# Kernel tuning notes

Measured on AMD Instinct MI355X. Metric: run time of the kernel, lower is better.

Reference implementation:

```python
import jax, jax.numpy as jnp
import numpy as np

D_MODEL, D_STATE, D_INNER, DT_RANK, K = 64, 16, 128, 4, 4
EPS = 1e-6  # RMSNorm eps


def setup_inputs() -> dict:
    key = jax.random.key(0)
    ks = jax.random.split(key, 12)
    B, L = 8, 4096
    s = 0.02
    x = jax.random.normal(ks[0], (B, L, D_MODEL), dtype=jnp.float32)
    w_norm = jnp.ones((D_MODEL,), jnp.float32)
    W_in = jax.random.normal(ks[1], (2 * D_INNER, D_MODEL), jnp.float32) * s
    b_in = jnp.zeros((2 * D_INNER,), jnp.float32)
    W_conv = jax.random.normal(ks[2], (D_INNER, D_INNER, K), jnp.float32) * s
    b_conv = jnp.zeros((D_INNER,), jnp.float32)
    W_xp = jax.random.normal(ks[3], (DT_RANK + 2 * D_STATE, D_INNER), jnp.float32) * s
    b_xp = jnp.zeros((DT_RANK + 2 * D_STATE,), jnp.float32)
    W_dt = jax.random.normal(ks[4], (D_INNER, DT_RANK), jnp.float32) * s
    b_dt = jnp.zeros((D_INNER,), jnp.float32)
    W_out = jax.random.normal(ks[5], (D_MODEL, D_INNER), jnp.float32) * s
    b_out = jnp.zeros((D_MODEL,), jnp.float32)
    A_log = jnp.log(jnp.tile(jnp.arange(1, D_STATE + 1, dtype=jnp.float32), (D_INNER, 1)))
    D_param = jnp.ones((D_INNER,), jnp.float32)
    return dict(x=x, w_norm=w_norm, W_in=W_in, b_in=b_in, W_conv=W_conv, b_conv=b_conv,
                W_xp=W_xp, b_xp=b_xp, W_dt=W_dt, b_dt=b_dt, W_out=W_out, b_out=b_out,
                A_log=A_log, D_param=D_param)


def _mamba_block(xn, W_in, b_in, W_conv, b_conv, W_xp, b_xp, W_dt, b_dt, W_out, b_out, A_log, D_param):
    B, L, _ = xn.shape
    xz = xn @ W_in.T + b_in                      # (B,L,2*d_inner)
    u, z = jnp.split(xz, 2, axis=-1)
    z = jax.nn.silu(z)
    # conv1d: NCH, causal-style pad (K-1) both sides then truncate to L
    uc = jax.lax.conv_general_dilated(
        u.transpose(0, 2, 1), W_conv, window_strides=(1,), padding=[(K - 1, K - 1)],
        dimension_numbers=("NCH", "OIH", "NCH"))[:, :, :L] + b_conv[None, :, None]
    u = jax.nn.silu(uc.transpose(0, 2, 1))       # (B,L,d_inner)
    xp = u @ W_xp.T + b_xp
    dt, Bm, Cm = jnp.split(xp, [DT_RANK, DT_RANK + D_STATE], axis=-1)
    delta = jax.nn.softplus(dt @ W_dt.T + b_dt)  # (B,L,d_inner)
    A = -jnp.exp(A_log)                          # (d_inner, n)
    A_bar = jnp.exp(jnp.einsum('bld,dn->bldn', delta, A))
    B_bar_x = jnp.einsum('bld,bln,bld->bldn', delta, Bm, u)

    def step(h, inp):
        a, bx, c = inp                           # (B,d,n),(B,d,n),(B,n)
        h = a * h + bx
        y = jnp.einsum('bdn,bn->bd', h, c)
        return h, y

    h0 = jnp.zeros((B, D_INNER, D_STATE), xn.dtype)
    xs = (A_bar.transpose(1, 0, 2, 3), B_bar_x.transpose(1, 0, 2, 3), Cm.transpose(1, 0, 2))
    _, ys = jax.lax.scan(step, h0, xs)           # (L,B,d_inner)
    y = ys.transpose(1, 0, 2) + D_param * u
    y = y * z
    return y @ W_out.T + b_out


def reference(x, w_norm, W_in, b_in, W_conv, b_conv, W_xp, b_xp, W_dt, b_dt, W_out, b_out, A_log, D_param):
    xn = x * jax.lax.rsqrt(jnp.mean(x * x, axis=-1, keepdims=True) + EPS) * w_norm
    return x + _mamba_block(xn, W_in, b_in, W_conv, b_conv, W_xp, b_xp, W_dt, b_dt, W_out, b_out, A_log, D_param)
```

## Files before the change

### kernel.cpp

```cpp
#include <hip/hip_runtime.h>
#include <math.h>

#define D_MODEL 64
#define D_STATE 16
#define D_INNER 128
#define DT_RANK 4
#define BB 8
#define LL 4096
#define NTOK (BB*LL)
#define EPSV 1e-6f
#define NCHUNK 64
#define LC (LL/NCHUNK)
#define PAD 136

typedef __attribute__((ext_vector_type(8))) short bf16x8;
typedef __attribute__((ext_vector_type(4))) float f32x4;

__device__ __forceinline__ float sig_(float v) { return 1.f / (1.f + __expf(-v)); }
__device__ __forceinline__ float softplus_(float v) {
    return (v > 20.f) ? v : __logf(1.f + __expf(v));
}
__device__ __forceinline__ unsigned short f2bf(float x) {
    unsigned int u = __float_as_uint(x);
    u += 0x7fff + ((u >> 16) & 1);
    return (unsigned short)(u >> 16);
}
__device__ __forceinline__ float bf2f(unsigned short u) {
    return __uint_as_float(((unsigned int)u) << 16);
}
__device__ __forceinline__ unsigned int pack2bf(float a, float b) {
    return (unsigned int)f2bf(a) | ((unsigned int)f2bf(b) << 16);
}

__global__ __launch_bounds__(256) void pack_all(
    const float* __restrict__ W_in, const float* __restrict__ w_norm,
    const float* __restrict__ W_conv, const float* __restrict__ W_xp,
    const float* __restrict__ W_out,
    unsigned short* __restrict__ Win_bf, unsigned short* __restrict__ Bp,
    unsigned short* __restrict__ Wxp_bf, unsigned short* __restrict__ Wout_bf)
{
    int i = blockIdx.x * 256 + threadIdx.x;
    if (i < 16384) {
        Win_bf[i] = f2bf(W_in[i] * w_norm[i & 63]);
    } else if (i < 81920) {
        int j = i - 16384;
        int kk = j >> 14, o = (j >> 7) & 127, c = j & 127;
        Bp[j] = f2bf(W_conv[o * 512 + c * 4 + kk]);
    } else if (i < 88064) {
        int j = i - 81920;
        Wxp_bf[j] = ((j >> 7) < 36) ? f2bf(W_xp[j]) : (unsigned short)0;
    } else if (i < 96256) {
        int j = i - 88064;
        Wout_bf[j] = f2bf(W_out[j]);
    }
}

__global__ __launch_bounds__(256) void k123a_fused(
    const float* __restrict__ x, const unsigned short* __restrict__ Win_bf,
    const float* __restrict__ b_in,
    const unsigned short* __restrict__ Bp, const float* __restrict__ b_conv,
    const unsigned short* __restrict__ Wxp_bf, const float* __restrict__ b_xp,
    const float* __restrict__ W_dt, const float* __restrict__ b_dt,
    const float* __restrict__ A_log,
    unsigned short* __restrict__ z_bf, unsigned short* __restrict__ u_cbf,
    unsigned short* __restrict__ delta_bf,
    float* __restrict__ Bm, float* __restrict__ Cm,
    float* __restrict__ P, float* __restrict__ Q)
{
    __shared__ unsigned char smem[54832];
    unsigned short* axs  = (unsigned short*)smem;
    unsigned short* upre = (unsigned short*)(smem + 11520);
    unsigned short* dls  = upre;
    unsigned short* uls  = (unsigned short*)(smem + 29744);
    float* bls = (float*)(smem + 47152);
    float (*dts)[4] = (float(*)[4])(smem + 51248);
    float* Wd  = (float*)(smem + 52272);
    float* bds = (float*)(smem + 54320);

    int tid = threadIdx.x;
    if (tid < 128) *(float4*)&Wd[tid * 4] = *(const float4*)&W_dt[tid * 4];
    else if (tid < 160) *(float4*)&bds[(tid - 128) * 4] = *(const float4*)&b_dt[(tid - 128) * 4];
    int wave = tid >> 6, lane = tid & 63;
    int quad = lane >> 4, l16 = lane & 15;
    int tb = blockIdx.x * 64;
    int bbase = tb & ~4095;

    #pragma unroll
    for (int p = 0; p < 2; ++p) {
        int lrow = p * 64 + (tid >> 2);
        if (lrow < 67) {
            int qt = tid & 3;
            int g = tb - 3 + lrow;
            float4 v[4];
            float ss = 0.f;
            if (g >= bbase) {
                #pragma unroll
                for (int j = 0; j < 4; ++j) {
                    v[j] = *(const float4*)&x[g * 64 + qt * 16 + j * 4];
                    ss += v[j].x*v[j].x + v[j].y*v[j].y + v[j].z*v[j].z + v[j].w*v[j].w;
                }
            } else {
                #pragma unroll
                for (int j = 0; j < 4; ++j) v[j] = (float4){0.f, 0.f, 0.f, 0.f};
            }
            ss += __shfl_xor(ss, 1, 64);
            ss += __shfl_xor(ss, 2, 64);
            float r = rsqrtf(ss * (1.f / 64.f) + EPSV);
            unsigned short tmp[16];
            #pragma unroll
            for (int j = 0; j < 4; ++j) {
                tmp[4*j+0] = f2bf(v[j].x * r); tmp[4*j+1] = f2bf(v[j].y * r);
                tmp[4*j+2] = f2bf(v[j].z * r); tmp[4*j+3] = f2bf(v[j].w * r);
            }
            *(bf16x8*)&axs[lrow * 72 + qt * 16]     = *(bf16x8*)&tmp[0];
            *(bf16x8*)&axs[lrow * 72 + qt * 16 + 8] = *(bf16x8*)&tmp[8];
        }
    }
    __syncthreads();
    #pragma unroll
    for (int mt = 0; mt < 5; ++mt) {
        bf16x8 a0 = *(const bf16x8*)&axs[(mt * 16 + l16) * 72 + quad * 8];
        bf16x8 a1 = *(const bf16x8*)&axs[(mt * 16 + l16) * 72 + 32 + quad * 8];
        f32x4 acc[4];
        #pragma unroll
        for (int nk = 0; nk < 4; ++nk) acc[nk] = (f32x4){0.f, 0.f, 0.f, 0.f};
        #pragma unroll
        for (int nk = 0; nk < 4; ++nk) {
            int nt = wave * 4 + nk;
            bf16x8 b0 = *(const bf16x8*)&Win_bf[(nt * 16 + l16) * 64 + quad * 8];
            bf16x8 b1 = *(const bf16x8*)&Win_bf[(nt * 16 + l16) * 64 + 32 + quad * 8];
            acc[nk] = __builtin_amdgcn_mfma_f32_16x16x32_bf16(a0, b0, acc[nk], 0, 0, 0);
            acc[nk] = __builtin_amdgcn_mfma_f32_16x16x32_bf16(a1, b1, acc[nk], 0, 0, 0);
        }
        #pragma unroll
        for (int nk = 0; nk < 4; ++nk) {
            int o = (wave * 4 + nk) * 16 + l16;
            float bo = b_in[o];
            #pragma unroll
            for (int r = 0; r < 4; ++r) {
                int lrow = mt * 16 + quad * 4 + r;
                if (lrow < 67) {
                    float v = acc[nk][r] + bo;
                    if (o < 128) {
                        upre[lrow * PAD + o] = f2bf(v);
                    } else if (lrow >= 3) {
                        float zv = v * sig_(v);
                        z_bf[(tb + lrow - 3) * 128 + (o - 128)] = f2bf(zv);
                    }
                }
            }
        }
    }
    __syncthreads();
    {
        f32x4 acc[8];
        #pragma unroll
        for (int og = 0; og < 8; ++og) acc[og] = (f32x4){0.f, 0.f, 0.f, 0.f};
        #pragma unroll
        for (int kk = 0; kk < 4; ++kk) {
            int lr = wave * 16 + l16 + kk;
            #pragma unroll
            for (int cs = 0; cs < 4; ++cs) {
                int kbase = cs * 32 + quad * 8;
                bf16x8 a = *(const bf16x8*)&upre[lr * PAD + kbase];
                #pragma unroll
                for (int og = 0; og < 8; ++og) {
                    bf16x8 b = *(const bf16x8*)&Bp[kk * 16384 + (og * 16 + l16) * 128 + kbase];
                    acc[og] = __builtin_amdgcn_mfma_f32_16x16x32_bf16(a, b, acc[og], 0, 0, 0);
                }
            }
        }
        #pragma unroll
        for (int og = 0; og < 8; ++og) {
            int o = og * 16 + l16;
            float bc = b_conv[o];
            #pragma unroll
            for (int r = 0; r < 4; ++r) {
                int tloc = wave * 16 + quad * 4 + r;
                float v = acc[og][r] + bc;
                unsigned short ub = f2bf(v * sig_(v));
                u_cbf[(tb + tloc) * 128 + o] = ub;
                uls[tloc * PAD + o] = ub;
            }
        }
    }
    __syncthreads();
    {
        f32x4 xacc[3];
        #pragma unroll
        for (int nt = 0; nt < 3; ++nt) xacc[nt] = (f32x4){0.f, 0.f, 0.f, 0.f};
        #pragma unroll
        for (int cs = 0; cs < 4; ++cs) {
            int kbase = cs * 32 + quad * 8;
            bf16x8 a = *(const bf16x8*)&uls[(wave * 16 + l16) * PAD + kbase];
            #pragma unroll
            for (int nt = 0; nt < 3; ++nt) {
                bf16x8 b = *(const bf16x8*)&Wxp_bf[(nt * 16 + l16) * 128 + kbase];
                xacc[nt] = __builtin_amdgcn_mfma_f32_16x16x32_bf16(a, b, xacc[nt], 0, 0, 0);
            }
        }
        #pragma unroll
        for (int nt = 0; nt < 3; ++nt) {
            int j = nt * 16 + l16;
            float bx = (j < 36) ? b_xp[j] : 0.f;
            #pragma unroll
            for (int r = 0; r < 4; ++r) {
                int tloc = wave * 16 + quad * 4 + r;
                int t = tb + tloc;
                float val = xacc[nt][r] + bx;
                if (j < 4) {
                    dts[tloc][j] = val;
                } else if (j < 20) {
                    Bm[t * 16 + (j - 4)] = val;
                    bls[tloc * 16 + (j - 4)] = val;
                } else if (j < 36) {
                    Cm[t * 16 + (j - 20)] = val;
                }
            }
        }
    }
    __syncthreads();
    {
        int tokloc = tid >> 2, dgrp = tid & 3;
        float dt0 = dts[tokloc][0], dt1 = dts[tokloc][1],
              dt2 = dts[tokloc][2], dt3 = dts[tokloc][3];
        int g = tb + tokloc;
        #pragma unroll
        for (int d4 = 0; d4 < 8; ++d4) {
            int d = dgrp * 32 + d4 * 4;
            float4 w0 = *(const float4*)&Wd[(d + 0) * 4];
            float4 w1 = *(const float4*)&Wd[(d + 1) * 4];
            float4 w2 = *(const float4*)&Wd[(d + 2) * 4];
            float4 w3 = *(const float4*)&Wd[(d + 3) * 4];
            float4 bdv = *(const float4*)&bds[d];
            float4 r;
            r.x = softplus_(bdv.x + dt0*w0.x + dt1*w0.y + dt2*w0.z + dt3*w0.w);
            r.y = softplus_(bdv.y + dt0*w1.x + dt1*w1.y + dt2*w1.z + dt3*w1.w);
            r.z = softplus_(bdv.z + dt0*w2.x + dt1*w2.y + dt2*w2.z + dt3*w2.w);
            r.w = softplus_(bdv.w + dt0*w3.x + dt1*w3.y + dt2*w3.z + dt3*w3.w);
            uint2 pk; pk.x = pack2bf(r.x, r.y); pk.y = pack2bf(r.z, r.w);
            *(uint2*)&delta_bf[g * 128 + d] = pk;
            *(uint2*)&dls[tokloc * PAD + d] = pk;
        }
    }
    __syncthreads();
    {
        int d = tid >> 1;
        int nb = (tid & 1) * 8;
        float4 Av0 = *(const float4*)&A_log[d * 16 + nb];
        float4 Av1 = *(const float4*)&A_log[d * 16 + nb + 4];
        float A0 = -__expf(Av0.x), A1 = -__expf(Av0.y),
              A2 = -__expf(Av0.z), A3 = -__expf(Av0.w);
        float A4 = -__expf(Av1.x), A5 = -__expf(Av1.y),
              A6 = -__expf(Av1.z), A7 = -__expf(Av1.w);
        float P0=1.f,P1=1.f,P2=1.f,P3=1.f,P4=1.f,P5=1.f,P6=1.f,P7=1.f;
        float Q0=0.f,Q1=0.f,Q2=0.f,Q3=0.f,Q4=0.f,Q5=0.f,Q6=0.f,Q7=0.f;
        for (int t = 0; t < LC; ++t) {
            float dl = bf2f(dls[t * PAD + d]);
            float uu = bf2f(uls[t * PAD + d]);
            float4 bm0 = *(const float4*)&bls[t * 16 + nb];
            float4 bm1 = *(const float4*)&bls[t * 16 + nb + 4];
            float du = dl * uu;
            float a0 = __expf(dl * A0), a1 = __expf(dl * A1),
                  a2 = __expf(dl * A2), a3 = __expf(dl * A3);
            float a4 = __expf(dl * A4), a5 = __expf(dl * A5),
                  a6 = __expf(dl * A6), a7 = __expf(dl * A7);
            P0 *= a0; P1 *= a1; P2 *= a2; P3 *= a3;
            P4 *= a4; P5 *= a5; P6 *= a6; P7 *= a7;
            Q0 = a0 * Q0 + du * bm0.x; Q1 = a1 * Q1 + du * bm0.y;
            Q2 = a2 * Q2 + du * bm0.z; Q3 = a3 * Q3 + du * bm0.w;
            Q4 = a4 * Q4 + du * bm1.x; Q5 = a5 * Q5 + du * bm1.y;
            Q6 = a6 * Q6 + du * bm1.z; Q7 = a7 * Q7 + du * bm1.w;
        }
        int idx = blockIdx.x * 2048 + d * 16 + nb;
        *(float4*)&P[idx]     = (float4){P0, P1, P2, P3};
        *(float4*)&P[idx + 4] = (float4){P4, P5, P6, P7};
        *(float4*)&Q[idx]     = (float4){Q0, Q1, Q2, Q3};
        *(float4*)&Q[idx + 4] = (float4){Q4, Q5, Q6, Q7};
    }
}

__global__ __launch_bounds__(256) void k4b_carry(
    const float* __restrict__ P, const float* __restrict__ Q, float* __restrict__ Hinit)
{
    int tid = blockIdx.x * 256 + threadIdx.x;
    int b = tid >> 11, dn = tid & 2047;
    float carry = 0.f;
    for (int c0 = 0; c0 < NCHUNK; c0 += 8) {
        float p[8], q[8];
        #pragma unroll
        for (int j = 0; j < 8; ++j) {
            int idx = (b * NCHUNK + c0 + j) * 2048 + dn;
            p[j] = P[idx]; q[j] = Q[idx];
        }
        #pragma unroll
        for (int j = 0; j < 8; ++j) {
            int idx = (b * NCHUNK + c0 + j) * 2048 + dn;
            Hinit[idx] = carry;
            carry = p[j] * carry + q[j];
        }
    }
}

__global__ __launch_bounds__(256) void k4c5_fused(
    const unsigned short* __restrict__ delta_bf, const unsigned short* __restrict__ u_cbf,
    const float* __restrict__ Bm, const float* __restrict__ Cm,
    const unsigned short* __restrict__ z_bf, const float* __restrict__ A_log,
    const float* __restrict__ D_param, const float* __restrict__ Hinit,
    const unsigned short* __restrict__ Wout_bf, const float* __restrict__ b_out,
    const float* __restrict__ x, float* __restrict__ out)
{
    __shared__ unsigned short dls[LC * 128];
    __shared__ unsigned short uls[LC * 128];
    __shared__ float bls[LC * 16];
    __shared__ float cls[LC * 16];
    __shared__ unsigned short yzls[LC * PAD];
    int bid = blockIdx.x;
    int tid = threadIdx.x, lane = tid & 63;
    int g0 = bid * 64;
    for (int i = tid; i < LC * 16; i += 256) {
        int row = i >> 4, q = i & 15;
        *(float4*)&dls[row * 128 + q * 8] =
            *(const float4*)&delta_bf[(g0 + row) * 128 + q * 8];
        *(float4*)&uls[row * 128 + q * 8] =
            *(const float4*)&u_cbf[(g0 + row) * 128 + q * 8];
        *(float4*)&yzls[row * PAD + q * 8] =
            *(const float4*)&z_bf[(g0 + row) * 128 + q * 8];
    }
    for (int i = tid; i < LC * 4; i += 256) {
        int row = i >> 2, q = i & 3;
        *(float4*)&bls[row * 16 + q * 4] = *(const float4*)&Bm[(g0 + row) * 16 + q * 4];
        *(float4*)&cls[row * 16 + q * 4] = *(const float4*)&Cm[(g0 + row) * 16 + q * 4];
    }
    int d = tid >> 1;
    int nb = (tid & 1) * 8;
    float4 Av0 = *(const float4*)&A_log[d * 16 + nb];
    float4 Av1 = *(const float4*)&A_log[d * 16 + nb + 4];
    float A0 = -__expf(Av0.x), A1 = -__expf(Av0.y), A2 = -__expf(Av0.z), A3 = -__expf(Av0.w);
    float A4 = -__expf(Av1.x), A5 = -__expf(Av1.y), A6 = -__expf(Av1.z), A7 = -__expf(Av1.w);
    int hbase = bid * 2048 + d * 16 + nb;
    float4 h0 = *(const float4*)&Hinit[hbase];
    float4 h1 = *(const float4*)&Hinit[hbase + 4];
    float Dp = D_param[d];
    __syncthreads();
    for (int t = 0; t < LC; ++t) {
        float dl = bf2f(dls[t * 128 + d]);
        float uu = bf2f(uls[t * 128 + d]);
        float4 bm0 = *(const float4*)&bls[t * 16 + nb];
        float4 bm1 = *(const float4*)&bls[t * 16 + nb + 4];
        float4 cm0 = *(const float4*)&cls[t * 16 + nb];
        float4 cm1 = *(const float4*)&cls[t * 16 + nb + 4];
        float du = dl * uu;
        float a0 = __expf(dl * A0), a1 = __expf(dl * A1),
              a2 = __expf(dl * A2), a3 = __expf(dl * A3);
        float a4 = __expf(dl * A4), a5 = __expf(dl * A5),
              a6 = __expf(dl * A6), a7 = __expf(dl * A7);
        h0.x = a0 * h0.x + du * bm0.x; h0.y = a1 * h0.y + du * bm0.y;
        h0.z = a2 * h0.z + du * bm0.z; h0.w = a3 * h0.w + du * bm0.w;
        h1.x = a4 * h1.x + du * bm1.x; h1.y = a5 * h1.y + du * bm1.y;
        h1.z = a6 * h1.z + du * bm1.z; h1.w = a7 * h1.w + du * bm1.w;
        float yv = h0.x * cm0.x + h0.y * cm0.y + h0.z * cm0.z + h0.w * cm0.w
                 + h1.x * cm1.x + h1.y * cm1.y + h1.z * cm1.z + h1.w * cm1.w;
        yv += __shfl_xor(yv, 1, 64);
        if ((tid & 1) == 0) {
            float y = yv + Dp * uu;
            y *= bf2f(yzls[t * PAD + d]);
            yzls[t * PAD + d] = f2bf(y);
        }
    }
    __syncthreads();
    int wave = tid >> 6;
    int quad = lane >> 4, l16 = lane & 15;
    f32x4 oacc[4];
    #pragma unroll
    for (int nt = 0; nt < 4; ++nt) oacc[nt] = (f32x4){0.f, 0.f, 0.f, 0.f};
    #pragma unroll
    for (int cs = 0; cs < 4; ++cs) {
        int kbase = cs * 32 + quad * 8;
        bf16x8 a = *(const bf16x8*)&yzls[(wave * 16 + l16) * PAD + kbase];
        #pragma unroll
        for (int nt = 0; nt < 4; ++nt) {
            bf16x8 bb = *(const bf16x8*)&Wout_bf[(nt * 16 + l16) * 128 + kbase];
            oacc[nt] = __builtin_amdgcn_mfma_f32_16x16x32_bf16(a, bb, oacc[nt], 0, 0, 0);
        }
    }
    #pragma unroll
    for (int nt = 0; nt < 4; ++nt) {
        int m = nt * 16 + l16;
        float bo = b_out[m];
        #pragma unroll
        for (int r = 0; r < 4; ++r) {
            int t = g0 + wave * 16 + quad * 4 + r;
            out[t * 64 + m] = oacc[nt][r] + bo + x[t * 64 + m];
        }
    }
}

extern "C" void kernel_launch(void* const* d_in, const int* in_sizes, int n_in,
                              void* d_out, int out_size, void* d_ws, size_t ws_size,
                              hipStream_t stream)
{
    const float* x       = (const float*)d_in[0];
    const float* w_norm  = (const float*)d_in[1];
    const float* W_in    = (const float*)d_in[2];
    const float* b_in    = (const float*)d_in[3];
    const float* W_conv  = (const float*)d_in[4];
    const float* b_conv  = (const float*)d_in[5];
    const float* W_xp    = (const float*)d_in[6];
    const float* b_xp    = (const float*)d_in[7];
    const float* W_dt    = (const float*)d_in[8];
    const float* b_dt    = (const float*)d_in[9];
    const float* W_out   = (const float*)d_in[10];
    const float* b_out   = (const float*)d_in[11];
    const float* A_log   = (const float*)d_in[12];
    const float* D_param = (const float*)d_in[13];
    float* ws = (float*)d_ws;

    unsigned short* z_bf     = (unsigned short*)ws;
    unsigned short* u_cbf    = (unsigned short*)(ws + 2097152);
    unsigned short* delta_bf = (unsigned short*)(ws + 4194304);
    float* Bm     = ws + 6291456;
    float* Cm     = ws + 6815744;
    float* P      = ws + 7340032;
    float* Q      = ws + 8388608;
    float* Hinit  = ws + 9437184;
    unsigned short* Bp      = (unsigned short*)(ws + 10485760);
    unsigned short* Wxp_bf  = (unsigned short*)(ws + 10518528);
    unsigned short* Wout_bf = (unsigned short*)(ws + 10521600);
    unsigned short* Win_bf  = (unsigned short*)(ws + 10525696);
    float* out    = (float*)d_out;

    pack_all<<<376, 256, 0, stream>>>(W_in, w_norm, W_conv, W_xp, W_out,
                                      Win_bf, Bp, Wxp_bf, Wout_bf);
    k123a_fused<<<512, 256, 0, stream>>>(x, Win_bf, b_in, Bp, b_conv,
                                         Wxp_bf, b_xp, W_dt, b_dt, A_log,
                                         z_bf, u_cbf, delta_bf, Bm, Cm, P, Q);
    k4b_carry<<<64, 256, 0, stream>>>(P, Q, Hinit);
    k4c5_fused<<<512, 256, 0, stream>>>(delta_bf, u_cbf, Bm, Cm, z_bf, A_log,
                                        D_param, Hinit, Wout_bf, b_out, x, out);
}
```

Baseline: 175.3 us.

## Fuse all mamba stages into one cooperative kernel with grid syncs

Replaces the three-kernel chain (projection/conv/chunk-scan, carry propagation, final scan plus output) with a single cooperative kernel that keeps u, delta, B and C in shared memory across a grid.sync. This removes the global round trips for u_cbf, delta_bf, Bm and Cm, along with two kernel launch boundaries. It needs all 512 blocks co-resident with about 64KB of LDS each. During the carry phase only 64 blocks do work while the rest wait at the grid barrier. If the cooperative launch fails, it falls back to the old three-kernel path.

```diff
diff --git a/kernel.cpp b/kernel.cpp
--- a/kernel.cpp
+++ b/kernel.cpp
@@ -1,5 +1,8 @@
 #include <hip/hip_runtime.h>
+#include <hip/hip_cooperative_groups.h>
 #include <math.h>
+
+namespace cg = cooperative_groups;
 
 #define D_MODEL 64
 #define D_STATE 16
@@ -52,6 +55,313 @@
     } else if (i < 96256) {
         int j = i - 88064;
         Wout_bf[j] = f2bf(W_out[j]);
+    }
+}
+
+__global__ __launch_bounds__(256) void mamba_coop(
+    const float* __restrict__ x, const unsigned short* __restrict__ Win_bf,
+    const float* __restrict__ b_in,
+    const unsigned short* __restrict__ Bp, const float* __restrict__ b_conv,
+    const unsigned short* __restrict__ Wxp_bf, const float* __restrict__ b_xp,
+    const float* __restrict__ W_dt, const float* __restrict__ b_dt,
+    const float* __restrict__ A_log, const float* __restrict__ D_param,
+    const unsigned short* __restrict__ Wout_bf, const float* __restrict__ b_out,
+    unsigned short* __restrict__ z_bf,
+    float* __restrict__ P, float* __restrict__ Q, float* __restrict__ Hinit,
+    float* __restrict__ out)
+{
+    __shared__ unsigned char smem[64816];
+    unsigned short* uls  = (unsigned short*)smem;
+    unsigned short* dlsu = (unsigned short*)(smem + 17408);
+    float* bls = (float*)(smem + 35632);
+    float* cls = (float*)(smem + 39728);
+    unsigned short* yzls = (unsigned short*)(smem + 43824);
+    unsigned short* axs  = yzls;
+    float (*dts)[4] = (float(*)[4])(smem + 61232);
+    float* Wd  = (float*)(smem + 62256);
+    float* bds = (float*)(smem + 64304);
+
+    cg::grid_group grid = cg::this_grid();
+    int tid = threadIdx.x;
+    if (tid < 128) *(float4*)&Wd[tid * 4] = *(const float4*)&W_dt[tid * 4];
+    else if (tid < 160) *(float4*)&bds[(tid - 128) * 4] = *(const float4*)&b_dt[(tid - 128) * 4];
+    int wave = tid >> 6, lane = tid & 63;
+    int quad = lane >> 4, l16 = lane & 15;
+    int bid = blockIdx.x;
+    int tb = bid * 64;
+    int bbase = tb & ~4095;
+
+    #pragma unroll
+    for (int p = 0; p < 2; ++p) {
+        int lrow = p * 64 + (tid >> 2);
+        if (lrow < 67) {
+            int qt = tid & 3;
+            int g = tb - 3 + lrow;
+            float4 v[4];
+            float ss = 0.f;
+            if (g >= bbase) {
+                #pragma unroll
+                for (int j = 0; j < 4; ++j) {
+                    v[j] = *(const float4*)&x[g * 64 + qt * 16 + j * 4];
+                    ss += v[j].x*v[j].x + v[j].y*v[j].y + v[j].z*v[j].z + v[j].w*v[j].w;
+                }
+            } else {
+                #pragma unroll
+                for (int j = 0; j < 4; ++j) v[j] = (float4){0.f, 0.f, 0.f, 0.f};
+            }
+            ss += __shfl_xor(ss, 1, 64);
+            ss += __shfl_xor(ss, 2, 64);
+            float r = rsqrtf(ss * (1.f / 64.f) + EPSV);
+            unsigned short tmp[16];
+            #pragma unroll
+            for (int j = 0; j < 4; ++j) {
+                tmp[4*j+0] = f2bf(v[j].x * r); tmp[4*j+1] = f2bf(v[j].y * r);
+                tmp[4*j+2] = f2bf(v[j].z * r); tmp[4*j+3] = f2bf(v[j].w * r);
+            }
+            *(bf16x8*)&axs[lrow * 72 + qt * 16]     = *(bf16x8*)&tmp[0];
+            *(bf16x8*)&axs[lrow * 72 + qt * 16 + 8] = *(bf16x8*)&tmp[8];
+        }
+    }
+    __syncthreads();
+    #pragma unroll
+    for (int mt = 0; mt < 5; ++mt) {
+        bf16x8 a0 = *(const bf16x8*)&axs[(mt * 16 + l16) * 72 + quad * 8];
+        bf16x8 a1 = *(const bf16x8*)&axs[(mt * 16 + l16) * 72 + 32 + quad * 8];
+        f32x4 acc[4];
+        #pragma unroll
+        for (int nk = 0; nk < 4; ++nk) acc[nk] = (f32x4){0.f, 0.f, 0.f, 0.f};
+        #pragma unroll
+        for (int nk = 0; nk < 4; ++nk) {
+            int nt = wave * 4 + nk;
+            bf16x8 b0 = *(const bf16x8*)&Win_bf[(nt * 16 + l16) * 64 + quad * 8];
+            bf16x8 b1 = *(const bf16x8*)&Win_bf[(nt * 16 + l16) * 64 + 32 + quad * 8];
+            acc[nk] = __builtin_amdgcn_mfma_f32_16x16x32_bf16(a0, b0, acc[nk], 0, 0, 0);
+            acc[nk] = __builtin_amdgcn_mfma_f32_16x16x32_bf16(a1, b1, acc[nk], 0, 0, 0);
+        }
+        #pragma unroll
+        for (int nk = 0; nk < 4; ++nk) {
+            int o = (wave * 4 + nk) * 16 + l16;
+            float bo = b_in[o];
+            #pragma unroll
+            for (int r = 0; r < 4; ++r) {
+                int lrow = mt * 16 + quad * 4 + r;
+                if (lrow < 67) {
+                    float v = acc[nk][r] + bo;
+                    if (o < 128) {
+                        dlsu[lrow * PAD + o] = f2bf(v);
+                    } else if (lrow >= 3) {
+                        float zv = v * sig_(v);
+                        z_bf[(tb + lrow - 3) * 128 + (o - 128)] = f2bf(zv);
+                    }
+                }
+            }
+        }
+    }
+    __syncthreads();
+    {
+        f32x4 acc[8];
+        #pragma unroll
+        for (int og = 0; og < 8; ++og) acc[og] = (f32x4){0.f, 0.f, 0.f, 0.f};
+        #pragma unroll
+        for (int kk = 0; kk < 4; ++kk) {
+            int lr = wave * 16 + l16 + kk;
+            #pragma unroll
+            for (int cs = 0; cs < 4; ++cs) {
+                int kbase = cs * 32 + quad * 8;
+                bf16x8 a = *(const bf16x8*)&dlsu[lr * PAD + kbase];
+                #pragma unroll
+                for (int og = 0; og < 8; ++og) {
+                    bf16x8 b = *(const bf16x8*)&Bp[kk * 16384 + (og * 16 + l16) * 128 + kbase];
+                    acc[og] = __builtin_amdgcn_mfma_f32_16x16x32_bf16(a, b, acc[og], 0, 0, 0);
+                }
+            }
+        }
+        __syncthreads();
+        #pragma unroll
+        for (int og = 0; og < 8; ++og) {
+            int o = og * 16 + l16;
+            float bc = b_conv[o];
+            #pragma unroll
+            for (int r = 0; r < 4; ++r) {
+                int tloc = wave * 16 + quad * 4 + r;
+                float v = acc[og][r] + bc;
+                uls[tloc * PAD + o] = f2bf(v * sig_(v));
+            }
+        }
+    }
+    __syncthreads();
+    {
+        f32x4 xacc[3];
+        #pragma unroll
+        for (int nt = 0; nt < 3; ++nt) xacc[nt] = (f32x4){0.f, 0.f, 0.f, 0.f};
+        #pragma unroll
+        for (int cs = 0; cs < 4; ++cs) {
+            int kbase = cs * 32 + quad * 8;
+            bf16x8 a = *(const bf16x8*)&uls[(wave * 16 + l16) * PAD + kbase];
+            #pragma unroll
+            for (int nt = 0; nt < 3; ++nt) {
+                bf16x8 b = *(const bf16x8*)&Wxp_bf[(nt * 16 + l16) * 128 + kbase];
+                xacc[nt] = __builtin_amdgcn_mfma_f32_16x16x32_bf16(a, b, xacc[nt], 0, 0, 0);
+            }
+        }
+        #pragma unroll
+        for (int nt = 0; nt < 3; ++nt) {
+            int j = nt * 16 + l16;
+            float bx = (j < 36) ? b_xp[j] : 0.f;
+            #pragma unroll
+            for (int r = 0; r < 4; ++r) {
+                int tloc = wave * 16 + quad * 4 + r;
+                float val = xacc[nt][r] + bx;
+                if (j < 4)       dts[tloc][j] = val;
+                else if (j < 20) bls[tloc * 16 + (j - 4)]  = val;
+                else if (j < 36) cls[tloc * 16 + (j - 20)] = val;
+            }
+        }
+    }
+    __syncthreads();
+    {
+        int tokloc = tid >> 2, dgrp = tid & 3;
+        float dt0 = dts[tokloc][0], dt1 = dts[tokloc][1],
+              dt2 = dts[tokloc][2], dt3 = dts[tokloc][3];
+        #pragma unroll
+        for (int d4 = 0; d4 < 8; ++d4) {
+            int d = dgrp * 32 + d4 * 4;
+            float4 w0 = *(const float4*)&Wd[(d + 0) * 4];
+            float4 w1 = *(const float4*)&Wd[(d + 1) * 4];
+            float4 w2 = *(const float4*)&Wd[(d + 2) * 4];
+            float4 w3 = *(const float4*)&Wd[(d + 3) * 4];
+            float4 bdv = *(const float4*)&bds[d];
+            float4 r;
+            r.x = softplus_(bdv.x + dt0*w0.x + dt1*w0.y + dt2*w0.z + dt3*w0.w);
+            r.y = softplus_(bdv.y + dt0*w1.x + dt1*w1.y + dt2*w1.z + dt3*w1.w);
+            r.z = softplus_(bdv.z + dt0*w2.x + dt1*w2.y + dt2*w2.z + dt3*w2.w);
+            r.w = softplus_(bdv.w + dt0*w3.x + dt1*w3.y + dt2*w3.z + dt3*w3.w);
+            uint2 pk; pk.x = pack2bf(r.x, r.y); pk.y = pack2bf(r.z, r.w);
+            *(uint2*)&dlsu[tokloc * PAD + d] = pk;
+        }
+    }
+    __syncthreads();
+    {
+        int d = tid >> 1;
+        int nb = (tid & 1) * 8;
+        float4 Av0 = *(const float4*)&A_log[d * 16 + nb];
+        float4 Av1 = *(const float4*)&A_log[d * 16 + nb + 4];
+        float A0 = -__expf(Av0.x), A1 = -__expf(Av0.y),
+              A2 = -__expf(Av0.z), A3 = -__expf(Av0.w);
+        float A4 = -__expf(Av1.x), A5 = -__expf(Av1.y),
+              A6 = -__expf(Av1.z), A7 = -__expf(Av1.w);
+        float P0=1.f,P1=1.f,P2=1.f,P3=1.f,P4=1.f,P5=1.f,P6=1.f,P7=1.f;
+        float Q0=0.f,Q1=0.f,Q2=0.f,Q3=0.f,Q4=0.f,Q5=0.f,Q6=0.f,Q7=0.f;
+        for (int t = 0; t < LC; ++t) {
+            float dl = bf2f(dlsu[t * PAD + d]);
+            float uu = bf2f(uls[t * PAD + d]);
+            float4 bm0 = *(const float4*)&bls[t * 16 + nb];
+            float4 bm1 = *(const float4*)&bls[t * 16 + nb + 4];
+            float du = dl * uu;
+            float a0 = __expf(dl * A0), a1 = __expf(dl * A1),
+                  a2 = __expf(dl * A2), a3 = __expf(dl * A3);
+            float a4 = __expf(dl * A4), a5 = __expf(dl * A5),
+                  a6 = __expf(dl * A6), a7 = __expf(dl * A7);
+            P0 *= a0; P1 *= a1; P2 *= a2; P3 *= a3;
+            P4 *= a4; P5 *= a5; P6 *= a6; P7 *= a7;
+            Q0 = a0 * Q0 + du * bm0.x; Q1 = a1 * Q1 + du * bm0.y;
+            Q2 = a2 * Q2 + du * bm0.z; Q3 = a3 * Q3 + du * bm0.w;
+            Q4 = a4 * Q4 + du * bm1.x; Q5 = a5 * Q5 + du * bm1.y;
+            Q6 = a6 * Q6 + du * bm1.z; Q7 = a7 * Q7 + du * bm1.w;
+        }
+        int idx = bid * 2048 + d * 16 + nb;
+        *(float4*)&P[idx]     = (float4){P0, P1, P2, P3};
+        *(float4*)&P[idx + 4] = (float4){P4, P5, P6, P7};
+        *(float4*)&Q[idx]     = (float4){Q0, Q1, Q2, Q3};
+        *(float4*)&Q[idx + 4] = (float4){Q4, Q5, Q6, Q7};
+    }
+    grid.sync();
+    if (bid < 64) {
+        int b = bid >> 3;
+        int dn = (bid & 7) * 256 + tid;
+        float carry = 0.f;
+        for (int c0 = 0; c0 < NCHUNK; c0 += 8) {
+            float p[8], q[8];
+            #pragma unroll
+            for (int j = 0; j < 8; ++j) {
+                int idx = (b * NCHUNK + c0 + j) * 2048 + dn;
+                p[j] = P[idx]; q[j] = Q[idx];
+            }
+            #pragma unroll
+            for (int j = 0; j < 8; ++j) {
+                int idx = (b * NCHUNK + c0 + j) * 2048 + dn;
+                Hinit[idx] = carry;
+                carry = p[j] * carry + q[j];
+            }
+        }
+    }
+    grid.sync();
+    for (int i = tid; i < LC * 16; i += 256) {
+        int row = i >> 4, q = i & 15;
+        *(float4*)&yzls[row * PAD + q * 8] =
+            *(const float4*)&z_bf[(tb + row) * 128 + q * 8];
+    }
+    int d = tid >> 1;
+    int nb = (tid & 1) * 8;
+    float4 Av0 = *(const float4*)&A_log[d * 16 + nb];
+    float4 Av1 = *(const float4*)&A_log[d * 16 + nb + 4];
+    float A0 = -__expf(Av0.x), A1 = -__expf(Av0.y), A2 = -__expf(Av0.z), A3 = -__expf(Av0.w);
+    float A4 = -__expf(Av1.x), A5 = -__expf(Av1.y), A6 = -__expf(Av1.z), A7 = -__expf(Av1.w);
+    int hbase = bid * 2048 + d * 16 + nb;
+    float4 h0 = *(const float4*)&Hinit[hbase];
+    float4 h1 = *(const float4*)&Hinit[hbase + 4];
+    float Dp = D_param[d];
+    __syncthreads();
+    for (int t = 0; t < LC; ++t) {
+        float dl = bf2f(dlsu[t * PAD + d]);
+        float uu = bf2f(uls[t * PAD + d]);
+        float4 bm0 = *(const float4*)&bls[t * 16 + nb];
+        float4 bm1 = *(const float4*)&bls[t * 16 + nb + 4];
+        float4 cm0 = *(const float4*)&cls[t * 16 + nb];
+        float4 cm1 = *(const float4*)&cls[t * 16 + nb + 4];
+        float du = dl * uu;
+        float a0 = __expf(dl * A0), a1 = __expf(dl * A1),
+              a2 = __expf(dl * A2), a3 = __expf(dl * A3);
+        float a4 = __expf(dl * A4), a5 = __expf(dl * A5),
+              a6 = __expf(dl * A6), a7 = __expf(dl * A7);
+        h0.x = a0 * h0.x + du * bm0.x; h0.y = a1 * h0.y + du * bm0.y;
+        h0.z = a2 * h0.z + du * bm0.z; h0.w = a3 * h0.w + du * bm0.w;
+        h1.x = a4 * h1.x + du * bm1.x; h1.y = a5 * h1.y + du * bm1.y;
+        h1.z = a6 * h1.z + du * bm1.z; h1.w = a7 * h1.w + du * bm1.w;
+        float yv = h0.x * cm0.x + h0.y * cm0.y + h0.z * cm0.z + h0.w * cm0.w
+                 + h1.x * cm1.x + h1.y * cm1.y + h1.z * cm1.z + h1.w * cm1.w;
+        yv += __shfl_xor(yv, 1, 64);
+        if ((tid & 1) == 0) {
+            float y = yv + Dp * uu;
+            y *= bf2f(yzls[t * PAD + d]);
+            yzls[t * PAD + d] = f2bf(y);
+        }
+    }
+    __syncthreads();
+    {
+        f32x4 oacc[4];
+        #pragma unroll
+        for (int nt = 0; nt < 4; ++nt) oacc[nt] = (f32x4){0.f, 0.f, 0.f, 0.f};
+        #pragma unroll
+        for (int cs = 0; cs < 4; ++cs) {
+            int kbase = cs * 32 + quad * 8;
+            bf16x8 a = *(const bf16x8*)&yzls[(wave * 16 + l16) * PAD + kbase];
+            #pragma unroll
+            for (int nt = 0; nt < 4; ++nt) {
+                bf16x8 bb = *(const bf16x8*)&Wout_bf[(nt * 16 + l16) * 128 + kbase];
+                oacc[nt] = __builtin_amdgcn_mfma_f32_16x16x32_bf16(a, bb, oacc[nt], 0, 0, 0);
+            }
+        }
+        #pragma unroll
+        for (int nt = 0; nt < 4; ++nt) {
+            int m = nt * 16 + l16;
+            float bo = b_out[m];
+            #pragma unroll
+            for (int r = 0; r < 4; ++r) {
+                int t = tb + wave * 16 + quad * 4 + r;
+                out[t * 64 + m] = oacc[nt][r] + bo + x[t * 64 + m];
+            }
+        }
     }
 }
 
@@ -432,10 +742,27 @@
 
     pack_all<<<376, 256, 0, stream>>>(W_in, w_norm, W_conv, W_xp, W_out,
                                       Win_bf, Bp, Wxp_bf, Wout_bf);
-    k123a_fused<<<512, 256, 0, stream>>>(x, Win_bf, b_in, Bp, b_conv,
-                                         Wxp_bf, b_xp, W_dt, b_dt, A_log,
-                                         z_bf, u_cbf, delta_bf, Bm, Cm, P, Q);
-    k4b_carry<<<64, 256, 0, stream>>>(P, Q, Hinit);
-    k4c5_fused<<<512, 256, 0, stream>>>(delta_bf, u_cbf, Bm, Cm, z_bf, A_log,
-                                        D_param, Hinit, Wout_bf, b_out, x, out);
-}
+
+    void* args[] = {
+        (void*)&x, (void*)&Win_bf, (void*)&b_in,
+        (void*)&Bp, (void*)&b_conv,
+        (void*)&Wxp_bf, (void*)&b_xp,
+        (void*)&W_dt, (void*)&b_dt,
+        (void*)&A_log, (void*)&D_param,
+        (void*)&Wout_bf, (void*)&b_out,
+        (void*)&z_bf,
+        (void*)&P, (void*)&Q, (void*)&Hinit,
+        (void*)&out,
+    };
+    hipError_t err = hipLaunchCooperativeKernel((const void*)mamba_coop,
+                                                dim3(512), dim3(256),
+                                                args, 0, stream);
+    if (err != hipSuccess) {
+        k123a_fused<<<512, 256, 0, stream>>>(x, Win_bf, b_in, Bp, b_conv,
+                                             Wxp_bf, b_xp, W_dt, b_dt, A_log,
+                                             z_bf, u_cbf, delta_bf, Bm, Cm, P, Q);
+        k4b_carry<<<64, 256, 0, stream>>>(P, Q, Hinit);
+        k4c5_fused<<<512, 256, 0, stream>>>(delta_bf, u_cbf, Bm, Cm, z_bf, A_log,
+                                            D_param, Hinit, Wout_bf, b_out, x, out);
+    }
+}
```

After: 308.9 us. +76.2%, slower.
